# Performance work log

Measured on AMD Instinct MI355X. Metric: run time of the kernel, lower is better.

Reference implementation:

```python
import jax, jax.numpy as jnp
import numpy as np

B, N1, N2, DIM = 16, 1024, 4096, 512
EPS_BN = 1e-5   # torch BatchNorm1d default eps
EPS_FP = 1e-8   # PointNet++ FP inverse-distance eps


def setup_inputs() -> dict:
    key = jax.random.key(0)
    ks = jax.random.split(key, 6)
    s1 = 1.0 / np.sqrt(2 * DIM)
    s2 = 1.0 / np.sqrt(DIM)
    return {
        "xyz1": jax.random.normal(ks[0], (B, N1, 3), jnp.float32),
        "points1": jax.random.normal(ks[1], (B, N1, 2 * DIM), jnp.float32),
        "xyz2": jax.random.normal(ks[2], (B, N2, 3), jnp.float32),
        "points2": jax.random.normal(ks[3], (B, N2, DIM), jnp.float32),
        "fc1_w": jax.random.normal(ks[4], (2 * DIM, DIM), jnp.float32) * s1,
        "fc1_b": jnp.zeros((DIM,), jnp.float32),
        "bn1_gamma": jnp.ones((DIM,), jnp.float32),
        "bn1_beta": jnp.zeros((DIM,), jnp.float32),
        "fc2_w": jax.random.normal(ks[5], (DIM, DIM), jnp.float32) * s2,
        "fc2_b": jnp.zeros((DIM,), jnp.float32),
        "bn2_gamma": jnp.ones((DIM,), jnp.float32),
        "bn2_beta": jnp.zeros((DIM,), jnp.float32),
    }


def _bn_relu(x, gamma, beta):
    # BatchNorm1d (training mode, batch stats) over (B, L) per channel; x is [B, L, C]
    mu = jnp.mean(x, axis=(0, 1), keepdims=True)
    var = jnp.var(x, axis=(0, 1), keepdims=True)
    return jax.nn.relu((x - mu) * jax.lax.rsqrt(var + EPS_BN) * gamma + beta)


def _fp_interpolate(xyz_dst, xyz_src, feats_src):
    # PointNet++ inverse-distance 3-NN interpolation.
    # xyz_dst [B,N,3], xyz_src [B,S,3], feats_src [B,S,C] -> [B,N,C]
    d = (jnp.sum(xyz_dst * xyz_dst, -1)[:, :, None]
         + jnp.sum(xyz_src * xyz_src, -1)[:, None, :]
         - 2.0 * jnp.einsum('bnd,bsd->bns', xyz_dst, xyz_src))  # squared dists [B,N,S]
    neg_d3, idx3 = jax.lax.top_k(-d, 3)                          # 3 smallest dists
    w = 1.0 / (-neg_d3 + EPS_FP)                                  # [B,N,3]
    w = w / jnp.sum(w, -1, keepdims=True)
    # gather: [B,1,S,C] indexed along axis 2 by [B,N,3,1] -> [B,N,3,C]
    gathered = jnp.take_along_axis(feats_src[:, None, :, :], idx3[..., None], axis=2)
    return jnp.einsum('bnkc,bnk->bnc', gathered, w)


def reference(xyz1, points1, xyz2, points2,
              fc1_w, fc1_b, bn1_gamma, bn1_beta,
              fc2_w, fc2_b, bn2_gamma, bn2_beta):
    feats1 = _bn_relu(points1 @ fc1_w + fc1_b, bn1_gamma, bn1_beta)   # [B,N1,DIM]
    feats1 = _fp_interpolate(xyz2, xyz1, feats1)                      # [B,N2,DIM]
    feats2 = _bn_relu(points2 @ fc2_w + fc2_b, bn2_gamma, bn2_beta)   # [B,N2,DIM]
    return (xyz2, feats1 + feats2)
```

## Files before the change

kernel.cpp:

```cpp
#include <hip/hip_runtime.h>
#include <stdint.h>

typedef unsigned short u16;
typedef __attribute__((ext_vector_type(8))) short short8;
typedef __attribute__((ext_vector_type(4))) float floatx4;

#define BB 16
#define NN1 1024
#define NN2 4096
#define DIM 512
#define M1 (BB*NN1)
#define M2 (BB*NN2)

__device__ __forceinline__ float bf2f(u16 u){
  union { unsigned int i; float f; } v; v.i = ((unsigned int)u) << 16; return v.f;
}
__device__ __forceinline__ u16 f2bf(float f){
  union { float f; unsigned int i; } v; v.f = f;
  unsigned int i = v.i;
  return (u16)((i + 0x7FFFu + ((i >> 16) & 1u)) >> 16);
}

__global__ void zero_stats(float* p){
  p[blockIdx.x * 256 + threadIdx.x] = 0.0f;
}

__global__ void transpose_w(const float* __restrict__ src, u16* __restrict__ dst,
                            int K, int N){
  int idx = blockIdx.x * 256 + threadIdx.x;
  if (idx < K * N){
    int n = idx / K, k = idx % K;
    dst[idx] = f2bf(src[k * N + n]);
  }
}

__global__ __launch_bounds__(256) void gemm_mfma(
    const float* __restrict__ A, const u16* __restrict__ BT,
    const float* __restrict__ bias, void* __restrict__ Yv,
    int M, int K, int out_is_f32,
    float* __restrict__ sum, float* __restrict__ sumsq)
{
  const int N = 512;
  __shared__ u16 As[128 * 32];
  __shared__ u16 Bs[128 * 32];
  int tid  = threadIdx.x;
  int lane = tid & 63, wave = tid >> 6;

  int id = blockIdx.x;
  int bm = (id & 7) + ((id >> 5) << 3);
  int bn = (id >> 3) & 3;

  int wm = (wave & 1) * 64, wn = (wave >> 1) * 64;
  int r16 = lane & 15, quad = lane >> 4;

  floatx4 acc[4][4];
  for (int i = 0; i < 4; i++)
    for (int j = 0; j < 4; j++)
      acc[i][j] = (floatx4)(0.0f);

  int lr = tid >> 2;
  int kc = tid & 3;

  const float* Ag = A  + (size_t)(bm * 128) * K;
  const u16*   Bg = BT + (size_t)(bn * 128) * K;

  int rsw = ((r16 >> 1) & 3) ^ quad;

  for (int k0 = 0; k0 < K; k0 += 32){
    for (int rr = 0; rr < 2; rr++){
      int row = lr + rr * 64;
      const float* ap = Ag + (size_t)row * K + k0 + kc * 8;
      float4 a0 = *(const float4*)ap;
      float4 a1 = *(const float4*)(ap + 4);
      u16 t[8] = { f2bf(a0.x), f2bf(a0.y), f2bf(a0.z), f2bf(a0.w),
                   f2bf(a1.x), f2bf(a1.y), f2bf(a1.z), f2bf(a1.w) };
      int dst = row * 32 + ((kc ^ ((row >> 1) & 3)) * 8);
      *(uint4*)(&As[dst]) = *(const uint4*)t;
      uint4 vb = *(const uint4*)(Bg + (size_t)row * K + k0 + kc * 8);
      *(uint4*)(&Bs[dst]) = vb;
    }
    __syncthreads();
    short8 af[4], bfr[4];
    for (int i = 0; i < 4; i++) af[i]  = *(const short8*)(&As[(wm + i*16 + r16) * 32 + rsw * 8]);
    for (int j = 0; j < 4; j++) bfr[j] = *(const short8*)(&Bs[(wn + j*16 + r16) * 32 + rsw * 8]);
    for (int i = 0; i < 4; i++)
      for (int j = 0; j < 4; j++)
        acc[i][j] = __builtin_amdgcn_mfma_f32_16x16x32_bf16(af[i], bfr[j], acc[i][j], 0, 0, 0);
    __syncthreads();
  }

  float cs[4] = {0.f, 0.f, 0.f, 0.f};
  float cq[4] = {0.f, 0.f, 0.f, 0.f};
  for (int i = 0; i < 4; i++){
    int rowb = bm * 128 + wm + i * 16 + quad * 4;
    for (int j = 0; j < 4; j++){
      int col = bn * 128 + wn + j * 16 + r16;
      float bv = bias[col];
      for (int r = 0; r < 4; r++){
        float v = acc[i][j][r] + bv;
        cs[j] += v; cq[j] += v * v;
        size_t idx = (size_t)(rowb + r) * N + col;
        if (out_is_f32) ((float*)Yv)[idx] = v;
        else            ((u16*)Yv)[idx]   = f2bf(v);
      }
    }
  }

  for (int j = 0; j < 4; j++){
    cs[j] += __shfl_xor(cs[j], 16); cs[j] += __shfl_xor(cs[j], 32);
    cq[j] += __shfl_xor(cq[j], 16); cq[j] += __shfl_xor(cq[j], 32);
  }
  float* S = (float*)As;
  if (lane < 16){
    int wmh = wave & 1, wnh = wave >> 1;
    for (int j = 0; j < 4; j++){
      int c = wnh * 64 + j * 16 + r16;
      S[wmh * 256 + c]       = cs[j];
      S[wmh * 256 + 128 + c] = cq[j];
    }
  }
  __syncthreads();
  {
    int stat = tid >> 7, c = tid & 127;
    float v = S[stat * 128 + c] + S[256 + stat * 128 + c];
    float* dstp = stat ? sumsq : sum;
    atomicAdd(&dstp[bn * 128 + c], v);
  }
}

__global__ void bn_coeff(const float* __restrict__ stats,
                         const float* __restrict__ g1, const float* __restrict__ be1,
                         const float* __restrict__ g2, const float* __restrict__ be2,
                         float* __restrict__ coef){
  int c = threadIdx.x;
  {
    float mu  = stats[c] / (float)M1;
    float var = stats[512 + c] / (float)M1 - mu * mu;
    var = fmaxf(var, 0.0f);
    float a = g1[c] * (1.0f / sqrtf(var + 1e-5f));
    coef[c] = a;
    coef[512 + c] = be1[c] - mu * a;
  }
  {
    float mu  = stats[1024 + c] / (float)M2;
    float var = stats[1536 + c] / (float)M2 - mu * mu;
    var = fmaxf(var, 0.0f);
    float a = g2[c] * (1.0f / sqrtf(var + 1e-5f));
    coef[1024 + c] = a;
    coef[1536 + c] = be2[c] - mu * a;
  }
}

__global__ void copy_xyz(const uint4* __restrict__ src, uint4* __restrict__ dst){
  int i = blockIdx.x * 256 + threadIdx.x;
  dst[i] = src[i];
}

__global__ __launch_bounds__(64) void interp_final(
    const float* __restrict__ xyz1, const float* __restrict__ xyz2,
    const u16* __restrict__ Y1, const float* __restrict__ coef,
    float* __restrict__ outF)
{
  int lane = threadIdx.x;
  int bid  = blockIdx.x;
  int b = bid >> 12;

  const float* pd = xyz2 + (size_t)bid * 3;
  double xd = (double)pd[0];
  double yd = (double)pd[1];
  double zd = (double)pd[2];

  double dl[16];
  const float* ps = xyz1 + (size_t)b * NN1 * 3;
  for (int s = 0; s < 16; s++){
    const float* q = ps + (s * 64 + lane) * 3;
    double dx = xd - (double)q[0];
    double dy = yd - (double)q[1];
    double dz = zd - (double)q[2];
    dl[s] = dx * dx + dy * dy + dz * dz;
  }

  double dsel[3]; int isel[3];
  for (int p = 0; p < 3; p++){
    double dm = dl[0]; int sm = 0;
    for (int s = 1; s < 16; s++) if (dl[s] < dm){ dm = dl[s]; sm = s; }
    int im = sm * 64 + lane;
    for (int off = 1; off < 64; off <<= 1){
      double od = __shfl_xor(dm, off);
      int    oi = __shfl_xor(im, off);
      if (od < dm || (od == dm && oi < im)){ dm = od; im = oi; }
    }
    dsel[p] = dm; isel[p] = im;
    if ((im & 63) == lane) dl[im >> 6] = 1e300;
  }

  double w0 = 1.0 / (dsel[0] + 1e-8);
  double w1 = 1.0 / (dsel[1] + 1e-8);
  double w2 = 1.0 / (dsel[2] + 1e-8);
  double wsum = w0 + w1 + w2;
  float f0 = (float)(w0 / wsum), f1 = (float)(w1 / wsum), f2 = (float)(w2 / wsum);

  const u16* r0 = Y1 + (size_t)(b * NN1 + isel[0]) * DIM;
  const u16* r1 = Y1 + (size_t)(b * NN1 + isel[1]) * DIM;
  const u16* r2 = Y1 + (size_t)(b * NN1 + isel[2]) * DIM;
  float* o = outF + (size_t)bid * DIM;

  int c0 = lane * 8;
  uint4 q0 = *(const uint4*)(r0 + c0);
  uint4 q1 = *(const uint4*)(r1 + c0);
  uint4 q2 = *(const uint4*)(r2 + c0);
  float4 ylo = *(const float4*)(o + c0);
  float4 yhi = *(const float4*)(o + c0 + 4);
  const u16* p0 = (const u16*)&q0;
  const u16* p1 = (const u16*)&q1;
  const u16* p2 = (const u16*)&q2;
  float yv[8] = { ylo.x, ylo.y, ylo.z, ylo.w, yhi.x, yhi.y, yhi.z, yhi.w };
  float res[8];
  for (int j = 0; j < 8; j++){
    int c = c0 + j;
    float a1 = coef[c],        b1 = coef[512 + c];
    float a2 = coef[1024 + c], b2 = coef[1536 + c];
    float v0 = fmaxf(a1 * bf2f(p0[j]) + b1, 0.0f);
    float v1 = fmaxf(a1 * bf2f(p1[j]) + b1, 0.0f);
    float v2 = fmaxf(a1 * bf2f(p2[j]) + b1, 0.0f);
    float vi = f0 * v0 + f1 * v1 + f2 * v2;
    float y2 = fmaxf(a2 * yv[j] + b2, 0.0f);
    res[j] = vi + y2;
  }
  *(float4*)(o + c0)     = make_float4(res[0], res[1], res[2], res[3]);
  *(float4*)(o + c0 + 4) = make_float4(res[4], res[5], res[6], res[7]);
}

extern "C" void kernel_launch(void* const* d_in, const int* in_sizes, int n_in,
                              void* d_out, int out_size, void* d_ws, size_t ws_size,
                              hipStream_t stream){
  const float* xyz1    = (const float*)d_in[0];
  const float* points1 = (const float*)d_in[1];
  const float* xyz2    = (const float*)d_in[2];
  const float* points2 = (const float*)d_in[3];
  const float* fc1_w   = (const float*)d_in[4];
  const float* fc1_b   = (const float*)d_in[5];
  const float* bn1_g   = (const float*)d_in[6];
  const float* bn1_b   = (const float*)d_in[7];
  const float* fc2_w   = (const float*)d_in[8];
  const float* fc2_b   = (const float*)d_in[9];
  const float* bn2_g   = (const float*)d_in[10];
  const float* bn2_b   = (const float*)d_in[11];

  char* ws = (char*)d_ws;
  u16*   Y1    = (u16*)(ws);
  u16*   wT1   = (u16*)(ws + 16777216);
  u16*   wT2   = (u16*)(ws + 17825792);
  float* stats = (float*)(ws + 18350080);
  float* coef  = (float*)(ws + 18358272);

  float* out  = (float*)d_out;
  float* outF = out + 196608;

  zero_stats<<<8, 256, 0, stream>>>(stats);
  transpose_w<<<(1024*512 + 255)/256, 256, 0, stream>>>(fc1_w, wT1, 1024, 512);
  transpose_w<<<( 512*512 + 255)/256, 256, 0, stream>>>(fc2_w, wT2,  512, 512);

  gemm_mfma<<<512, 256, 0, stream>>>(points1, wT1, fc1_b, Y1,   M1, 1024, 0,
                                     stats,        stats + 512);
  gemm_mfma<<<2048, 256, 0, stream>>>(points2, wT2, fc2_b, outF, M2,  512, 1,
                                      stats + 1024, stats + 1536);

  bn_coeff<<<1, 512, 0, stream>>>(stats, bn1_g, bn1_b, bn2_g, bn2_b, coef);

  copy_xyz<<<192, 256, 0, stream>>>((const uint4*)xyz2, (uint4*)out);
  interp_final<<<65536, 64, 0, stream>>>(xyz1, xyz2, Y1, coef, outF);
}
```

Measured before the change: 478.8 us.

## Merge small prep kernels, load B tiles directly to LDS, use packed bf16 convert

Folds the stats zeroing and both weight transposes into one prep kernel, and the BN coefficient computation and xyz copy into one kernel, which cuts launch overhead. In the GEMM, the bf16 weight tile is now loaded straight into LDS with global_load_lds, skipping the trip through registers. The fp32-to-bf16 conversion of A now uses the packed v_cvt_pk_bf16_f32 instruction. The swizzled LDS layout for B must match the fragment read pattern, and the direct-to-LDS load depends on correct wave-based destination addressing.

```diff
diff --git a/kernel.cpp b/kernel.cpp
--- a/kernel.cpp
+++ b/kernel.cpp
@@ -21,16 +21,30 @@
   return (u16)((i + 0x7FFFu + ((i >> 16) & 1u)) >> 16);
 }
 
-__global__ void zero_stats(float* p){
-  p[blockIdx.x * 256 + threadIdx.x] = 0.0f;
-}
-
-__global__ void transpose_w(const float* __restrict__ src, u16* __restrict__ dst,
-                            int K, int N){
+__device__ __forceinline__ uint32_t cvtpk(float lo, float hi){
+  uint32_t r;
+  asm("v_cvt_pk_bf16_f32 %0, %1, %2" : "=v"(r) : "v"(lo), "v"(hi));
+  return r;
+}
+
+__device__ __forceinline__ void gload_lds16(const void* g, void* l){
+  __builtin_amdgcn_global_load_lds(
+      (const __attribute__((address_space(1))) void*)g,
+      (__attribute__((address_space(3))) void*)l, 16, 0, 0);
+}
+
+__global__ void prep(const float* __restrict__ fc1_w, const float* __restrict__ fc2_w,
+                     u16* __restrict__ wT1, u16* __restrict__ wT2,
+                     float* __restrict__ stats){
   int idx = blockIdx.x * 256 + threadIdx.x;
-  if (idx < K * N){
-    int n = idx / K, k = idx % K;
-    dst[idx] = f2bf(src[k * N + n]);
+  if (idx < 2048) stats[idx] = 0.0f;
+  if (idx < 512 * 1024){
+    int n = idx >> 10, k = idx & 1023;
+    wT1[idx] = f2bf(fc1_w[k * 512 + n]);
+  } else {
+    int j = idx - 512 * 1024;
+    int n = j >> 9, k = j & 511;
+    wT2[j] = f2bf(fc2_w[k * 512 + n]);
   }
 }
 
@@ -64,20 +78,32 @@
   const float* Ag = A  + (size_t)(bm * 128) * K;
   const u16*   Bg = BT + (size_t)(bn * 128) * K;
 
+  int pb0 = wave * 128 + lane;
+  int rb0 = pb0 >> 2, cb0 = (pb0 & 3) ^ ((rb0 >> 1) & 3);
+  int pb1 = pb0 + 64;
+  int rb1 = pb1 >> 2, cb1 = (pb1 & 3) ^ ((rb1 >> 1) & 3);
+  const u16* bsrc0 = Bg + (size_t)rb0 * K + cb0 * 8;
+  const u16* bsrc1 = Bg + (size_t)rb1 * K + cb1 * 8;
+  u16* bdst0 = &Bs[(wave * 128) * 8];
+  u16* bdst1 = &Bs[(wave * 128 + 64) * 8];
+
   int rsw = ((r16 >> 1) & 3) ^ quad;
 
   for (int k0 = 0; k0 < K; k0 += 32){
+    gload_lds16(bsrc0 + k0, bdst0);
+    gload_lds16(bsrc1 + k0, bdst1);
     for (int rr = 0; rr < 2; rr++){
       int row = lr + rr * 64;
       const float* ap = Ag + (size_t)row * K + k0 + kc * 8;
       float4 a0 = *(const float4*)ap;
       float4 a1 = *(const float4*)(ap + 4);
-      u16 t[8] = { f2bf(a0.x), f2bf(a0.y), f2bf(a0.z), f2bf(a0.w),
-                   f2bf(a1.x), f2bf(a1.y), f2bf(a1.z), f2bf(a1.w) };
+      uint4 tv;
+      tv.x = cvtpk(a0.x, a0.y);
+      tv.y = cvtpk(a0.z, a0.w);
+      tv.z = cvtpk(a1.x, a1.y);
+      tv.w = cvtpk(a1.z, a1.w);
       int dst = row * 32 + ((kc ^ ((row >> 1) & 3)) * 8);
-      *(uint4*)(&As[dst]) = *(const uint4*)t;
-      uint4 vb = *(const uint4*)(Bg + (size_t)row * K + k0 + kc * 8);
-      *(uint4*)(&Bs[dst]) = vb;
+      *(uint4*)(&As[dst]) = tv;
     }
     __syncthreads();
     short8 af[4], bfr[4];
@@ -128,32 +154,34 @@
   }
 }
 
-__global__ void bn_coeff(const float* __restrict__ stats,
-                         const float* __restrict__ g1, const float* __restrict__ be1,
-                         const float* __restrict__ g2, const float* __restrict__ be2,
-                         float* __restrict__ coef){
-  int c = threadIdx.x;
-  {
-    float mu  = stats[c] / (float)M1;
-    float var = stats[512 + c] / (float)M1 - mu * mu;
-    var = fmaxf(var, 0.0f);
-    float a = g1[c] * (1.0f / sqrtf(var + 1e-5f));
-    coef[c] = a;
-    coef[512 + c] = be1[c] - mu * a;
-  }
-  {
-    float mu  = stats[1024 + c] / (float)M2;
-    float var = stats[1536 + c] / (float)M2 - mu * mu;
-    var = fmaxf(var, 0.0f);
-    float a = g2[c] * (1.0f / sqrtf(var + 1e-5f));
-    coef[1024 + c] = a;
-    coef[1536 + c] = be2[c] - mu * a;
-  }
-}
-
-__global__ void copy_xyz(const uint4* __restrict__ src, uint4* __restrict__ dst){
-  int i = blockIdx.x * 256 + threadIdx.x;
-  dst[i] = src[i];
+__global__ void bn_coeff_copy(const float* __restrict__ stats,
+                              const float* __restrict__ g1, const float* __restrict__ be1,
+                              const float* __restrict__ g2, const float* __restrict__ be2,
+                              float* __restrict__ coef,
+                              const uint4* __restrict__ xsrc, uint4* __restrict__ xdst){
+  int b = blockIdx.x, tid = threadIdx.x;
+  if (b == 0){
+    int c = tid;
+    {
+      float mu  = stats[c] / (float)M1;
+      float var = stats[512 + c] / (float)M1 - mu * mu;
+      var = fmaxf(var, 0.0f);
+      float a = g1[c] * (1.0f / sqrtf(var + 1e-5f));
+      coef[c] = a;
+      coef[512 + c] = be1[c] - mu * a;
+    }
+    {
+      float mu  = stats[1024 + c] / (float)M2;
+      float var = stats[1536 + c] / (float)M2 - mu * mu;
+      var = fmaxf(var, 0.0f);
+      float a = g2[c] * (1.0f / sqrtf(var + 1e-5f));
+      coef[1024 + c] = a;
+      coef[1536 + c] = be2[c] - mu * a;
+    }
+  } else {
+    int i = (b - 1) * 512 + tid;
+    xdst[i] = xsrc[i];
+  }
 }
 
 __global__ __launch_bounds__(64) void interp_final(
@@ -257,17 +285,15 @@
   float* out  = (float*)d_out;
   float* outF = out + 196608;
 
-  zero_stats<<<8, 256, 0, stream>>>(stats);
-  transpose_w<<<(1024*512 + 255)/256, 256, 0, stream>>>(fc1_w, wT1, 1024, 512);
-  transpose_w<<<( 512*512 + 255)/256, 256, 0, stream>>>(fc2_w, wT2,  512, 512);
+  prep<<<3072, 256, 0, stream>>>(fc1_w, fc2_w, wT1, wT2, stats);
 
   gemm_mfma<<<512, 256, 0, stream>>>(points1, wT1, fc1_b, Y1,   M1, 1024, 0,
                                      stats,        stats + 512);
   gemm_mfma<<<2048, 256, 0, stream>>>(points2, wT2, fc2_b, outF, M2,  512, 1,
                                       stats + 1024, stats + 1536);
 
-  bn_coeff<<<1, 512, 0, stream>>>(stats, bn1_g, bn1_b, bn2_g, bn2_b, coef);
-
-  copy_xyz<<<192, 256, 0, stream>>>((const uint4*)xyz2, (uint4*)out);
+  bn_coeff_copy<<<97, 512, 0, stream>>>(stats, bn1_g, bn1_b, bn2_g, bn2_b, coef,
+                                        (const uint4*)xyz2, (uint4*)out);
+
   interp_final<<<65536, 64, 0, stream>>>(xyz1, xyz2, Y1, coef, outF);
 }
```

Result: faster. 465.0 us (-2.9%).
